# Kernel optimization log

Hardware: AMD Instinct MI355X
Metric: run time of the kernel (lower is better)

## Reference

```python
import jax, jax.numpy as jnp
import numpy as np
import math

EPS = 1e-5
N_HEADS = 4


def _ln(x, g, b):
    mu = jnp.mean(x, axis=-1, keepdims=True)
    var = jnp.mean((x - mu) ** 2, axis=-1, keepdims=True)
    return (x - mu) * jax.lax.rsqrt(var + EPS) * g + b


def _eq_ln(s, v, g, b, vscale):
    # scalar LayerNorm + equivariant vector norm rescaling
    s = _ln(s, g, b)
    vn = jnp.sqrt(jnp.sum(v * v, axis=-1, keepdims=True))  # (B,N,C,1)
    v = v / (vn + EPS) * jnp.mean(vn, axis=-2, keepdims=True) * vscale[None, None, :, None]
    return s, v


def _block(s, v, pos, Wq, bq, Wk, bk, Wv, bv, Wo, bo, w_dist, b_dist, Wvv, Wvo,
           g1, be1, vs1, g2, be2, vs2, Wf1, bf1, Wf2, bf2, Wfv1, Wfv2):
    B, N, S = s.shape
    D = S // N_HEADS
    # --- norm1 + attention ---
    sn, vn = _eq_ln(s, v, g1, be1, vs1)
    q = (sn @ Wq + bq).reshape(B, N, N_HEADS, D)
    k = (sn @ Wk + bk).reshape(B, N, N_HEADS, D)
    vs = (sn @ Wv + bv).reshape(B, N, N_HEADS, D)
    attn = jnp.einsum('bnhd,bmhd->bhnm', q, k) / math.sqrt(D)
    # pairwise Euclidean distance via the |x|^2 + |y|^2 - 2xy trick (clamped for sqrt safety)
    p2 = jnp.sum(pos * pos, axis=-1)  # (B,N)
    d2 = p2[:, :, None] + p2[:, None, :] - 2.0 * jnp.einsum('bnd,bmd->bnm', pos, pos)
    dist = jnp.sqrt(jnp.maximum(d2, 1e-12))  # (B,N,N)
    # dist_proj: Linear(1 -> n_heads) + Softplus, applied per pair
    bias = jax.nn.softplus(dist[..., None] * w_dist + b_dist)  # (B,N,N,H)
    attn = jax.nn.softmax(attn - jnp.transpose(bias, (0, 3, 1, 2)), axis=-1)  # (B,H,N,N)
    attn_mean = jnp.mean(attn, axis=1)  # (B,N,N)
    s_attn = jnp.einsum('bhnm,bmhd->bnhd', attn, vs).reshape(B, N, S) @ Wo + bo
    # vector channel mixing + rotation by head-averaged attention
    v_mix = jnp.einsum('bncx,ce->bnex', vn, Wvv)          # (B,N,C,3)
    v_attn = jnp.einsum('bnm,bmcx->bncx', attn_mean, v_mix)
    v_attn = jnp.einsum('bncx,ce->bnex', v_attn, Wvo)
    s = s + s_attn
    v = v + v_attn
    # --- norm2 + FFN ---
    sn, vn = _eq_ln(s, v, g2, be2, vs2)
    s = s + (jax.nn.gelu(sn @ Wf1 + bf1, approximate=False) @ Wf2 + bf2)
    v = v + jnp.einsum('bnhx,hc->bncx', jnp.einsum('bncx,ch->bnhx', vn, Wfv1), Wfv2)
    return s, v


def setup_inputs() -> dict:
    B, N, S, C, H = 4, 2048, 256, 64, N_HEADS
    key = jax.random.key(0)
    ks = jax.random.split(key, 24)

    def nrm(k, shape, scale=0.02):
        return jax.random.normal(k, shape, dtype=jnp.float32) * scale

    return {
        's': jax.random.normal(ks[0], (B, N, S), dtype=jnp.float32),
        'v': jax.random.normal(ks[1], (B, N, C, 3), dtype=jnp.float32),
        'pos': jax.random.normal(ks[2], (B, N, 3), dtype=jnp.float32),
        'Wq': nrm(ks[3], (S, S)), 'bq': nrm(ks[4], (S,)),
        'Wk': nrm(ks[5], (S, S)), 'bk': nrm(ks[6], (S,)),
        'Wv': nrm(ks[7], (S, S)), 'bv': nrm(ks[8], (S,)),
        'Wo': nrm(ks[9], (S, S)), 'bo': nrm(ks[10], (S,)),
        'w_dist': nrm(ks[11], (H,), 0.5), 'b_dist': nrm(ks[12], (H,), 0.5),
        'Wvv': nrm(ks[13], (C, C)), 'Wvo': nrm(ks[14], (C, C)),
        'g1': jnp.ones((S,), jnp.float32), 'be1': jnp.zeros((S,), jnp.float32),
        'vs1': jnp.ones((C,), jnp.float32),
        'g2': jnp.ones((S,), jnp.float32), 'be2': jnp.zeros((S,), jnp.float32),
        'vs2': jnp.ones((C,), jnp.float32),
        'Wf1': nrm(ks[15], (S, 4 * S)), 'bf1': nrm(ks[16], (4 * S,)),
        'Wf2': nrm(ks[17], (4 * S, S)), 'bf2': nrm(ks[18], (S,)),
        'Wfv1': nrm(ks[19], (C, 4 * C)), 'Wfv2': nrm(ks[20], (4 * C, C)),
    }


def reference(s, v, pos, Wq, bq, Wk, bk, Wv, bv, Wo, bo, w_dist, b_dist, Wvv, Wvo,
              g1, be1, vs1, g2, be2, vs2, Wf1, bf1, Wf2, bf2, Wfv1, Wfv2):
    return _block(s, v, pos, Wq, bq, Wk, bk, Wv, bv, Wo, bo, w_dist, b_dist, Wvv, Wvo,
                  g1, be1, vs1, g2, be2, vs2, Wf1, bf1, Wf2, bf2, Wfv1, Wfv2)
```

## Files before the change

### kernel.cpp

```cpp
#include <hip/hip_runtime.h>
#include <hip/hip_bf16.h>

using bf16 = __hip_bfloat16;
typedef __attribute__((ext_vector_type(8))) short short8;
typedef __attribute__((ext_vector_type(4))) float float4v;
typedef __attribute__((ext_vector_type(16))) float f32x16;
typedef __attribute__((ext_vector_type(4))) unsigned uint4v;

__device__ __forceinline__ float b2f(bf16 x){ return __bfloat162float(x); }
__device__ __forceinline__ bf16  f2b(float x){ return __float2bfloat16(x); }
__device__ __forceinline__ bf16  tob(float x){ return f2b(x); }
__device__ __forceinline__ bf16  tob(bf16 x){ return x; }
__device__ __forceinline__ float frcp(float x){ return __builtin_amdgcn_rcpf(x); }
__device__ __forceinline__ float bs2f(short s){
  unsigned u = ((unsigned)(unsigned short)s) << 16;
  return __builtin_bit_cast(float, u);
}
__device__ __forceinline__ unsigned cvt_pk_bf16(float lo, float hi){
  unsigned r; asm("v_cvt_pk_bf16_f32 %0, %1, %2" : "=v"(r) : "v"(lo), "v"(hi)); return r;
}
__device__ __forceinline__ void plswap(unsigned &a, unsigned &b){
  asm("v_permlane32_swap_b32 %0, %1" : "+v"(a), "+v"(b));
}

#define EPSV 1e-5f
#define Z16 {0.f,0.f,0.f,0.f,0.f,0.f,0.f,0.f,0.f,0.f,0.f,0.f,0.f,0.f,0.f,0.f}

__global__ __launch_bounds__(256) void pos_kernel(const float* __restrict__ pos,
                                                  float* __restrict__ posf, int rows){
  int r = blockIdx.x*256 + threadIdx.x;
  if (r >= rows) return;
  float x = pos[3*r], y = pos[3*r+1], z = pos[3*r+2];
  posf[4*r] = x; posf[4*r+1] = y; posf[4*r+2] = z; posf[4*r+3] = x*x + y*y + z*z;
}

struct WTDesc { const float* src; bf16* dst; int rows, cols; };
struct WTPack { WTDesc d[10]; };

__global__ __launch_bounds__(256) void wtrans_kernel(WTPack p){
  WTDesc w = p.d[blockIdx.z];
  long r0 = (long)blockIdx.y*32, c0 = (long)blockIdx.x*32;
  if (r0 >= w.rows || c0 >= w.cols) return;
  __shared__ bf16 tile[32][33];
  int tx = threadIdx.x & 31, ty = threadIdx.x >> 5;
#pragma unroll
  for (int i = ty; i < 32; i += 8) tile[i][tx] = f2b(w.src[(r0+i)*w.cols + c0 + tx]);
  __syncthreads();
#pragma unroll
  for (int i = ty; i < 32; i += 8) w.dst[(c0+i)*w.rows + r0 + tx] = tile[tx][i];
}

template<typename TI>
__global__ __launch_bounds__(256) void transpose_kernel(
    const TI* __restrict__ in, long ldin, long is1, long is2,
    bf16* __restrict__ out, long ldout, long os1, long os2, int Z2)
{
  int z = blockIdx.z, z1 = z / Z2, z2 = z - z1*Z2;
  in  += (long)z1*is1 + (long)z2*is2;
  out += (long)z1*os1 + (long)z2*os2;
  __shared__ bf16 tile[32][33];
  int tx = threadIdx.x & 31, ty = threadIdx.x >> 5;
  long r0 = (long)blockIdx.y*32, c0 = (long)blockIdx.x*32;
#pragma unroll
  for (int i = ty; i < 32; i += 8) tile[i][tx] = tob(in[(r0+i)*ldin + c0 + tx]);
  __syncthreads();
#pragma unroll
  for (int i = ty; i < 32; i += 8) out[(c0+i)*ldout + r0 + tx] = tile[tx][i];
}

__global__ __launch_bounds__(256) void bcat_kernel(const float* __restrict__ bq,
                                                   const float* __restrict__ bk,
                                                   const float* __restrict__ bv,
                                                   float* __restrict__ bqkv){
  int j = blockIdx.x*256 + threadIdx.x;
  if (j >= 768) return;
  bqkv[j] = (j < 256) ? bq[j] : (j < 512) ? bk[j-256] : bv[j-512];
}

__global__ __launch_bounds__(256) void ln_kernel(const float* __restrict__ x,
                                                 const float* __restrict__ g,
                                                 const float* __restrict__ be,
                                                 bf16* __restrict__ out){
  const long row = blockIdx.x;
  const int t = threadIdx.x;
  __shared__ float r1[256], r2[256];
  float v = x[(row<<8) + t];
  r1[t] = v; r2[t] = v*v; __syncthreads();
  for (int s=128;s>0;s>>=1){
    if (t<s){ r1[t] += r1[t+s]; r2[t] += r2[t+s]; }
    __syncthreads();
  }
  const float mu = r1[0] * (1.f/256.f);
  const float var = r2[0] * (1.f/256.f) - mu*mu;
  const float rstd = rsqrtf(fmaxf(var, 0.f) + EPSV);
  out[(row<<8)+t] = f2b((v-mu)*rstd*g[t] + be[t]);
}

__global__ __launch_bounds__(192) void vnorm1_kernel(const float* __restrict__ vin,
                                                     const float* __restrict__ vs1,
                                                     bf16* __restrict__ vnX){
  const long row = blockIdx.x;
  const int t = threadIdx.x;
  __shared__ float vv[192], nrm[64];
  __shared__ float smean;
  vv[t] = vin[row*192 + t];
  __syncthreads();
  if (t < 64){
    float a = vv[3*t], b = vv[3*t+1], c = vv[3*t+2];
    nrm[t] = sqrtf(a*a + b*b + c*c);
  }
  __syncthreads();
  if (t == 0){ float s = 0.f; for (int i=0;i<64;i++) s += nrm[i]; smean = s*(1.f/64.f); }
  __syncthreads();
  const int c = t/3, x = t - 3*c;
  const float val = vv[t] / (nrm[c] + EPSV) * smean * vs1[c];
  vnX[row*192 + x*64 + c] = f2b(val);
}

__global__ __launch_bounds__(192) void vnorm2_kernel(const float* __restrict__ v2X,
                                                     const float* __restrict__ vs2,
                                                     bf16* __restrict__ vn2X){
  const long row = blockIdx.x;
  const int t = threadIdx.x;
  __shared__ float vv[192], nrm[64];
  __shared__ float smean;
  vv[t] = v2X[row*192 + t];
  __syncthreads();
  if (t < 64){
    float a = vv[t], b = vv[t+64], c = vv[t+128];
    nrm[t] = sqrtf(a*a + b*b + c*c);
  }
  __syncthreads();
  if (t == 0){ float s = 0.f; for (int i=0;i<64;i++) s += nrm[i]; smean = s*(1.f/64.f); }
  __syncthreads();
  const int c = t & 63;
  vn2X[row*192 + t] = f2b(vv[t] / (nrm[c] + EPSV) * smean * vs2[c]);
}

__global__ __launch_bounds__(256) void knorm_kernel(const bf16* __restrict__ qkv,
                                                    float* __restrict__ kmax){
  const int bh = blockIdx.x, b = bh>>2, h = bh&3;
  const int t = threadIdx.x;
  __shared__ float red[256];
  float mx = 0.f;
  for (int r=0;r<8;r++){
    long row = (long)b*2048 + r*256 + t;
    const short8* kp = (const short8*)(qkv + row*768 + 256 + h*64);
    float ss = 0.f;
#pragma unroll
    for (int c=0;c<8;c++){
      short8 v = kp[c];
#pragma unroll
      for (int j=0;j<8;j++){ float f = bs2f(v[j]); ss = fmaf(f,f,ss); }
    }
    mx = fmaxf(mx, ss);
  }
  red[t] = mx; __syncthreads();
  for (int s=128;s>0;s>>=1){ if (t<s) red[t] = fmaxf(red[t], red[t+s]); __syncthreads(); }
  if (t==0) kmax[bh] = sqrtf(red[0]);
}

#define ATT_K_OFF   0
#define ATT_V_OFF   4096
#define ATT_X_OFF   9216
#define ATT_P_OFF   24576
#define ATT_TILE    25088
#define ATT_GRP     50176
#define ATT_LACC    98304
#define ATT_SMEM    100352

__global__ __launch_bounds__(512, 2) void attn_kernel(
    const bf16* __restrict__ qkv,
    const bf16* __restrict__ vsT,
    const bf16* __restrict__ vmixT,
    const float* __restrict__ posf,
    const float* __restrict__ kmaxA,
    const float* __restrict__ w_dist, const float* __restrict__ b_dist,
    bf16* __restrict__ sA,
    bf16* __restrict__ slab)
{
  __shared__ __align__(16) char smem[ATT_SMEM];
  const int qb = blockIdx.x;
  const int bh = blockIdx.y;
  const int b  = bh >> 2, h = bh & 3;
  const int tid = threadIdx.x;
  const int w = tid >> 6, lane = tid & 63;
  const int g = w >> 2, qw = w & 3;
  const int lq = lane & 31, hi = lane >> 5;
  const int gtid = tid & 255;

  const int qloc = qb*128 + qw*32 + lq;
  const long rowQ = (long)b*2048 + qloc;

  short8 qf[4];
  {
    const bf16* qp = qkv + rowQ*768 + h*64 + hi*8;
#pragma unroll
    for (int kc=0;kc<4;kc++) qf[kc] = *(const short8*)(qp + kc*16);
  }
  float q2 = 0.f;
#pragma unroll
  for (int kc=0;kc<4;kc++)
#pragma unroll
    for (int j=0;j<8;j++){ float qv = bs2f(qf[kc][j]); q2 = fmaf(qv,qv,q2); }
  q2 += __shfl_xor(q2, 32);
  const float mxs = sqrtf(q2) * kmaxA[bh] * 0.125f;
  const float wh = w_dist[h], bhd = b_dist[h];
  const float4v pn = *(const float4v*)(posf + (long)b*8192 + (long)qloc*4);
  const float m2x = -2.f*pn[0], m2y = -2.f*pn[1], m2z = -2.f*pn[2], pnw = pn[3];

  f32x16 O[2]  = {Z16, Z16};
  f32x16 VM[6] = {Z16, Z16, Z16, Z16, Z16, Z16};
  float lacc = 0.f;

  short8 stK, stV, stX0, stX1, stX2; float4v stP;
  const int sm = gtid >> 3, sc = gtid & 7;
  const int vd = gtid >> 2, vc = gtid & 3;
  const bf16* Kg = qkv + (long)b*2048*768 + 256 + h*64;
  const bf16* Vg = vsT + (long)b*524288 + (long)h*131072;
  const bf16* Xg = vmixT + (long)b*393216;
  const float* Pg = posf + (long)b*8192;
  char* gbase = smem + g*ATT_GRP;

  auto LOADT = [&](int m0){
    stK  = *(const short8*)(Kg + (long)(m0+sm)*768 + sc*8);
    stV  = *(const short8*)(Vg + (long)vd*2048 + m0 + vc*8);
    stX0 = *(const short8*)(Xg + (long)vd*2048 + m0 + vc*8);
    stX1 = *(const short8*)(Xg + (long)(64+vd)*2048 + m0 + vc*8);
    stX2 = *(const short8*)(Xg + (long)(128+vd)*2048 + m0 + vc*8);
    if (gtid < 32) stP = *(const float4v*)(Pg + (long)(m0+gtid)*4);
  };
  auto WRITET = [&](char* buf){
    *(short8*)(buf + ATT_K_OFF + sm*128 + ((sc ^ (sm&7))<<4)) = stK;
    *(short8*)(buf + ATT_V_OFF + vd*80 + vc*16) = stV;
    *(short8*)(buf + ATT_X_OFF + vd*80 + vc*16) = stX0;
    *(short8*)(buf + ATT_X_OFF + (64+vd)*80 + vc*16) = stX1;
    *(short8*)(buf + ATT_X_OFF + (128+vd)*80 + vc*16) = stX2;
    if (gtid < 32) *(float4v*)(buf + ATT_P_OFF + gtid*16) = stP;
  };

  auto COMPUTE = [&](const char* buf){
    const char* Kb = buf + ATT_K_OFF;
    const char* Vb = buf + ATT_V_OFF;
    const char* Xb = buf + ATT_X_OFF;
    const float4v* pmb = (const float4v*)(buf + ATT_P_OFF);
    f32x16 S = Z16;
#pragma unroll
    for (int kc=0;kc<4;kc++){
      short8 kf = *(const short8*)(Kb + lq*128 + (((kc*2+hi) ^ (lq&7))<<4));
      S = __builtin_amdgcn_mfma_f32_32x32x16_bf16(kf, qf[kc], S, 0, 0, 0);
    }
    float P[16];
#pragma unroll
    for (int gg=0; gg<4; gg++){
#pragma unroll
      for (int i=0;i<4;i++){
        float4v pm = pmb[gg*8 + hi*4 + i];
        float d2 = fmaf(m2x, pm[0], fmaf(m2y, pm[1], fmaf(m2z, pm[2], pnw + pm[3])));
        float dist = sqrtf(fmaxf(d2, 1e-12f));
        float sig = frcp(1.f + __expf(fmaf(dist, wh, bhd)));
        float p = __expf(fmaf(S[gg*4+i], 0.125f, -mxs)) * sig;
        lacc += p;
        P[gg*4+i] = p;
      }
    }
    unsigned pk[8];
#pragma unroll
    for (int t=0;t<8;t++) pk[t] = cvt_pk_bf16(P[2*t], P[2*t+1]);
    plswap(pk[0], pk[2]); plswap(pk[1], pk[3]);
    plswap(pk[4], pk[6]); plswap(pk[5], pk[7]);
    uint4v y0v = {pk[0], pk[1], pk[2], pk[3]};
    uint4v y1v = {pk[4], pk[5], pk[6], pk[7]};
    short8 Y0 = __builtin_bit_cast(short8, y0v);
    short8 Y1 = __builtin_bit_cast(short8, y1v);
#pragma unroll
    for (int dblk=0; dblk<2; dblk++){
      short8 v0 = *(const short8*)(Vb + (dblk*32+lq)*80 + hi*16);
      short8 v1 = *(const short8*)(Vb + (dblk*32+lq)*80 + 32 + hi*16);
      O[dblk] = __builtin_amdgcn_mfma_f32_32x32x16_bf16(v0, Y0, O[dblk], 0,0,0);
      O[dblk] = __builtin_amdgcn_mfma_f32_32x32x16_bf16(v1, Y1, O[dblk], 0,0,0);
    }
#pragma unroll
    for (int eblk=0; eblk<6; eblk++){
      short8 x0 = *(const short8*)(Xb + (eblk*32+lq)*80 + hi*16);
      short8 x1 = *(const short8*)(Xb + (eblk*32+lq)*80 + 32 + hi*16);
      VM[eblk] = __builtin_amdgcn_mfma_f32_32x32x16_bf16(x0, Y0, VM[eblk], 0,0,0);
      VM[eblk] = __builtin_amdgcn_mfma_f32_32x32x16_bf16(x1, Y1, VM[eblk], 0,0,0);
    }
  };

  LOADT(g*32);
  WRITET(gbase);
  __syncthreads();
#pragma unroll 1
  for (int i=0; i<32; ++i){
    if (i < 31) LOADT((2*(i+1)+g)*32);
    COMPUTE(gbase + (i&1)*ATT_TILE);
    if (i < 31) WRITET(gbase + ((i+1)&1)*ATT_TILE);
    __syncthreads();
  }

  float* laccT = (float*)(smem + ATT_LACC);
  laccT[w*64 + lane] = lacc;
  if (g == 1){
    float* Od = (float*)(smem + ATT_GRP) + (qw*64+lane)*33;
#pragma unroll
    for (int r=0;r<16;r++){ Od[r] = O[0][r]; Od[16+r] = O[1][r]; }
  }
  __syncthreads();
  const float lsum = laccT[qw*64+lq] + laccT[qw*64+32+lq]
                   + laccT[(4+qw)*64+lq] + laccT[(4+qw)*64+32+lq];
  if (g == 0){
    const float* Od = (const float*)(smem + ATT_GRP) + (qw*64+lane)*33;
#pragma unroll
    for (int r=0;r<16;r++){ O[0][r] += Od[r]; O[1][r] += Od[16+r]; }
  }
  __syncthreads();
#pragma unroll
  for (int hf=0; hf<2; hf++){
    if (g == 0){
      float* Vd = (float*)smem + (qw*64+lane)*49;
#pragma unroll
      for (int e=0;e<3;e++)
#pragma unroll
        for (int r=0;r<16;r++) Vd[e*16+r] = VM[hf*3+e][r];
    }
    __syncthreads();
    if (g == 1){
      const float* Vd = (const float*)smem + (qw*64+lane)*49;
#pragma unroll
      for (int e=0;e<3;e++)
#pragma unroll
        for (int r=0;r<16;r++) VM[hf*3+e][r] += Vd[e*16+r];
    }
    __syncthreads();
  }

  const float sinv = frcp(lsum);
  if (g == 0){
    char* scr = smem + qw*12544;
#pragma unroll
    for (int dblk=0; dblk<2; dblk++)
#pragma unroll
      for (int pp=0; pp<8; pp++){
        const int r = 2*pp;
        const int d = dblk*32 + (r&3) + 8*(r>>2) + 4*hi;
        unsigned u = cvt_pk_bf16(O[dblk][r]*sinv, O[dblk][r+1]*sinv);
        *(unsigned*)(scr + lq*136 + d*2) = u;
      }
  } else {
    const float vinv = 0.25f * sinv;
    char* scr = smem + ATT_GRP + qw*12544;
#pragma unroll
    for (int eblk=0; eblk<6; eblk++)
#pragma unroll
      for (int pp=0; pp<8; pp++){
        const int r = 2*pp;
        const int e = eblk*32 + (r&3) + 8*(r>>2) + 4*hi;
        unsigned u = cvt_pk_bf16(VM[eblk][r]*vinv, VM[eblk][r+1]*vinv);
        *(unsigned*)(scr + lq*392 + e*2) = u;
      }
  }
  __syncthreads();
  if (g == 0){
    const char* scr = smem + qw*12544;
    const int q = lane >> 1, half = lane & 1;
    const char* src = scr + q*136 + half*64;
    char* dst = (char*)(sA + (long)(b*2048 + qb*128 + qw*32 + q)*256 + h*64 + half*32);
#pragma unroll
    for (int i=0;i<8;i++)
      *(unsigned long long*)(dst + i*8) = *(const unsigned long long*)(src + i*8);
  } else {
    const char* scr = smem + ATT_GRP + qw*12544;
    const int q = lane >> 1, half = lane & 1;
    const char* src = scr + q*392 + half*192;
    char* dst = (char*)(slab + (long)h*1572864
                        + (long)(b*2048 + qb*128 + qw*32 + q)*192 + half*96);
#pragma unroll
    for (int i=0;i<24;i++)
      *(unsigned long long*)(dst + i*8) = *(const unsigned long long*)(src + i*8);
  }
}

__global__ __launch_bounds__(256) void hred_kernel(const bf16* __restrict__ slab,
                                                   bf16* __restrict__ out){
  long i = (long)blockIdx.x*256 + threadIdx.x;
  if (i >= 196608) return;
  const short8* s0 = (const short8*)slab + i;
  short8 a = s0[0], b = s0[196608], c = s0[2*196608], d = s0[3*196608];
  short8 o;
#pragma unroll
  for (int j=0;j<8;j++){
    float f = bs2f(a[j]) + bs2f(b[j]) + bs2f(c[j]) + bs2f(d[j]);
    bf16 hv = f2b(f); o[j] = *(short*)&hv;
  }
  ((short8*)out)[i] = o;
}

template<int MT, int NT, int ACT, int OUTM, int RXIL, int CXIL, int SWZ>
__global__ __launch_bounds__(64) void gemm_kernel(
    const bf16* __restrict__ A, long lda, long As1, long As2,
    const bf16* __restrict__ BT, long ldb, long Bs1, long Bs2,
    const float* __restrict__ bias,
    const float* __restrict__ resid, long ldr, long Rs1, long Rs2,
    void* __restrict__ Cv, long ldc, long Cs1, long Cs2,
    int K, int Z2, int KS)
{
  int z = blockIdx.z;
  int zz = z / KS, ks = z - zz*KS;
  int z1 = zz / Z2, z2 = zz - z1*Z2;
  A  += (long)z1*As1 + (long)z2*As2 + (long)ks*K;
  BT += (long)z1*Bs1 + (long)z2*Bs2 + (long)ks*K;
  if (resid) resid += (long)z1*Rs1 + (long)z2*Rs2;
  const long cbase = (long)z1*Cs1 + (long)z2*Cs2;

  int bx = blockIdx.x, by = blockIdx.y;
  if (SWZ){
    const int nx = gridDim.x, ny = gridDim.y;
    long lin = (long)by*nx + bx;
    const int xcd = (int)(lin & 7);
    long idx = lin >> 3;
    const int rpx = ny >> 3;
    by = xcd*rpx + (int)(idx / nx);
    bx = (int)(idx % nx);
  }

  const int lane = threadIdx.x;
  const int col = lane & 15, quad = lane >> 4;
  const long rowA0 = (long)by*(16*MT);
  const long colB0 = (long)bx*(16*NT);

  float4v acc[MT][NT];
#pragma unroll
  for (int m=0;m<MT;m++)
#pragma unroll
    for (int n=0;n<NT;n++) acc[m][n] = (float4v){0.f,0.f,0.f,0.f};

  const bf16* ap[MT];
  const bf16* bp[NT];
#pragma unroll
  for (int m=0;m<MT;m++) ap[m] = A + (rowA0 + m*16 + col)*lda + quad*8;
#pragma unroll
  for (int n=0;n<NT;n++) bp[n] = BT + (colB0 + n*16 + col)*ldb + quad*8;

  for (int k0 = 0; k0 < K; k0 += 32){
    short8 a[MT], bb[NT];
#pragma unroll
    for (int m=0;m<MT;m++){ a[m] = *(const short8*)ap[m]; ap[m] += 32; }
#pragma unroll
    for (int n=0;n<NT;n++){ bb[n] = *(const short8*)bp[n]; bp[n] += 32; }
#pragma unroll
    for (int m=0;m<MT;m++)
#pragma unroll
      for (int n=0;n<NT;n++)
        acc[m][n] = __builtin_amdgcn_mfma_f32_16x16x32_bf16(a[m], bb[n], acc[m][n], 0, 0, 0);
  }

#pragma unroll
  for (int m=0;m<MT;m++){
    const long ri = rowA0 + m*16 + quad*4;
#pragma unroll
    for (int n=0;n<NT;n++){
      const long cj = colB0 + n*16 + col;
      const float bbias = bias ? bias[cj] : 0.f;
#pragma unroll
      for (int r=0;r<4;r++){
        const long ci = ri + r;
        float val = acc[m][n][r] + bbias;
        if (ACT == 1) val = 0.5f*val*(1.f + erff(val*0.70710678118654752f));
        if (resid){
          const long raddr = RXIL ? ((ci/3)*192 + cj*3 + (ci%3)) : (ci*ldr + cj);
          val += resid[raddr];
        }
        const long caddr = CXIL ? (cbase + (ci/3)*192 + cj*3 + (ci%3))
                                : (cbase + ci*ldc + cj);
        if (OUTM == 0)      ((bf16*)Cv)[caddr] = f2b(val);
        else if (OUTM == 1) ((float*)Cv)[caddr] = val;
        else                unsafeAtomicAdd(&((float*)Cv)[caddr], val);
      }
    }
  }
}

extern "C" void kernel_launch(void* const* d_in, const int* in_sizes, int n_in,
                              void* d_out, int out_size, void* d_ws, size_t ws_size,
                              hipStream_t stream)
{
  const float* s    = (const float*)d_in[0];
  const float* v    = (const float*)d_in[1];
  const float* pos  = (const float*)d_in[2];
  const float* Wq   = (const float*)d_in[3];
  const float* bq   = (const float*)d_in[4];
  const float* Wk   = (const float*)d_in[5];
  const float* bk   = (const float*)d_in[6];
  const float* Wv   = (const float*)d_in[7];
  const float* bv   = (const float*)d_in[8];
  const float* Wo   = (const float*)d_in[9];
  const float* bo   = (const float*)d_in[10];
  const float* w_d  = (const float*)d_in[11];
  const float* b_d  = (const float*)d_in[12];
  const float* Wvv  = (const float*)d_in[13];
  const float* Wvo  = (const float*)d_in[14];
  const float* g1   = (const float*)d_in[15];
  const float* be1  = (const float*)d_in[16];
  const float* vs1  = (const float*)d_in[17];
  const float* g2   = (const float*)d_in[18];
  const float* be2  = (const float*)d_in[19];
  const float* vs2  = (const float*)d_in[20];
  const float* Wf1  = (const float*)d_in[21];
  const float* bf1  = (const float*)d_in[22];
  const float* Wf2  = (const float*)d_in[23];
  const float* bf2  = (const float*)d_in[24];
  const float* Wfv1 = (const float*)d_in[25];
  const float* Wfv2 = (const float*)d_in[26];

  float* outS = (float*)d_out;
  float* outV = outS + (size_t)4*2048*256;

  char* w = (char*)d_ws;
  size_t o = 0;
  auto alloc = [&](size_t bytes)->char* {
    char* p = w + o;
    o = (o + bytes + 255) & ~(size_t)255;
    return p;
  };
  float* posf  = (float*)alloc(131072);
  bf16* WqkvT = (bf16*)alloc(393216);
  bf16* WoT   = (bf16*)alloc(131072);
  bf16* Wf1T  = (bf16*)alloc(524288);
  bf16* Wf2T  = (bf16*)alloc(524288);
  bf16* WvvT  = (bf16*)alloc(8192);
  bf16* WvoT  = (bf16*)alloc(8192);
  bf16* Wfv1T = (bf16*)alloc(32768);
  bf16* Wfv2T = (bf16*)alloc(32768);
  float* bqkv = (float*)alloc(3072);
  float* kmax = (float*)alloc(64);
  bf16* sn    = (bf16*)alloc(4194304);
  bf16* qkv   = (bf16*)alloc(12582912);
  bf16* vsT   = (bf16*)alloc(4194304);
  bf16* sA    = (bf16*)alloc(4194304);
  float* s2   = (float*)alloc(8388608);
  bf16* vnX   = (bf16*)alloc(3145728);
  bf16* vmixX = (bf16*)alloc(3145728);
  bf16* vmixXT= (bf16*)alloc(3145728);
  float* v2X  = (float*)alloc(6291456);
  bf16* slab  = (bf16*)alloc(12582912);
  bf16* h1    = (bf16*)alloc(16777216);
  bf16* vn2X  = vnX;
  bf16* tvXb  = vmixX;
  bf16* hv    = qkv;
  if (o > ws_size) return;

  pos_kernel<<<32, 256, 0, stream>>>(pos, posf, 8192);
  WTPack pk;
  pk.d[0] = {Wq,   WqkvT,          256, 256};
  pk.d[1] = {Wk,   WqkvT + 65536,  256, 256};
  pk.d[2] = {Wv,   WqkvT + 131072, 256, 256};
  pk.d[3] = {Wo,   WoT,            256, 256};
  pk.d[4] = {Wf1,  Wf1T,           256, 1024};
  pk.d[5] = {Wf2,  Wf2T,           1024, 256};
  pk.d[6] = {Wvv,  WvvT,           64, 64};
  pk.d[7] = {Wvo,  WvoT,           64, 64};
  pk.d[8] = {Wfv1, Wfv1T,          64, 256};
  pk.d[9] = {Wfv2, Wfv2T,          256, 64};
  wtrans_kernel<<<dim3(32,32,10), 256, 0, stream>>>(pk);
  bcat_kernel<<<3, 256, 0, stream>>>(bq, bk, bv, bqkv);

  ln_kernel<<<8192, 256, 0, stream>>>(s, g1, be1, sn);
  vnorm1_kernel<<<8192, 192, 0, stream>>>(v, vs1, vnX);

  gemm_kernel<2,4,0,0,0,0,0><<<dim3(1,768,1), 64, 0, stream>>>(vnX,64,0,0, WvvT,64,0,0,
      nullptr, nullptr,0,0,0, vmixX,64,0,0, 64, 1, 1);
  transpose_kernel<bf16><<<dim3(6,64,4), 256, 0, stream>>>(vmixX, 192, 393216,0,
      vmixXT, 2048, 393216,0, 1);

  gemm_kernel<2,4,0,0,0,0,1><<<dim3(12,256,1), 64, 0, stream>>>(sn,256,0,0, WqkvT,256,0,0,
      bqkv, nullptr,0,0,0, qkv,768,0,0, 256, 1, 1);
  transpose_kernel<bf16><<<dim3(2,64,16), 256, 0, stream>>>(qkv+512, 768, 1572864,64,
      vsT, 2048, 524288,131072, 4);

  knorm_kernel<<<16, 256, 0, stream>>>(qkv, kmax);
  attn_kernel<<<dim3(16,16), 512, 0, stream>>>(qkv, vsT, vmixXT, posf, kmax,
      w_d, b_d, sA, slab);
  hred_kernel<<<768, 256, 0, stream>>>(slab, tvXb);

  gemm_kernel<2,4,0,1,0,0,1><<<dim3(4,256,1), 64, 0, stream>>>(sA,256,0,0, WoT,256,0,0,
      bo, s,256,0,0, s2,256,0,0, 256, 1, 1);

  gemm_kernel<2,4,0,1,1,0,0><<<dim3(1,768,1), 64, 0, stream>>>(tvXb,64,0,0, WvoT,64,0,0,
      nullptr, v,0,0,0, v2X,64,0,0, 64, 1, 1);

  ln_kernel<<<8192, 256, 0, stream>>>(s2, g2, be2, sn);
  gemm_kernel<2,4,1,0,0,0,1><<<dim3(16,256,1), 64, 0, stream>>>(sn,256,0,0, Wf1T,256,0,0,
      bf1, nullptr,0,0,0, h1,1024,0,0, 256, 1, 1);
  gemm_kernel<2,4,0,1,0,0,1><<<dim3(4,256,1), 64, 0, stream>>>(h1,1024,0,0, Wf2T,1024,0,0,
      bf2, s2,256,0,0, outS,256,0,0, 1024, 1, 1);

  vnorm2_kernel<<<8192, 192, 0, stream>>>(v2X, vs2, vn2X);
  gemm_kernel<2,4,0,0,0,0,1><<<dim3(4,768,1), 64, 0, stream>>>(vn2X,64,0,0, Wfv1T,64,0,0,
      nullptr, nullptr,0,0,0, hv,256,0,0, 64, 1, 1);
  gemm_kernel<2,4,0,1,0,1,0><<<dim3(1,768,1), 64, 0, stream>>>(hv,256,0,0, Wfv2T,256,0,0,
      nullptr, v2X,64,0,0, outV,0,0,0, 256, 1, 1);
}
```

Measured before the change: 425.9 us.

## Shrink attention blocks, single-buffer tiles, parallelize knorm, enlarge GEMM tiles

The attention kernel moves from 512-thread blocks of 128 queries with double-buffered shared tiles to 256-thread blocks of 64 queries with a single buffer. This halves shared memory per block so more blocks can be resident, at the cost of an extra barrier per iteration and less load/compute overlap. The key-norm reduction is split across 8 row chunks per head and combined with an atomic max on squared norms, which are zeroed in the bias-concat kernel; the square root moves into the attention kernel. All GEMM launches switch to a larger M tile template parameter with half as many blocks.

```diff
diff --git a/kernel.cpp b/kernel.cpp
--- a/kernel.cpp
+++ b/kernel.cpp
@@ -71,8 +71,10 @@
 __global__ __launch_bounds__(256) void bcat_kernel(const float* __restrict__ bq,
                                                    const float* __restrict__ bk,
                                                    const float* __restrict__ bv,
-                                                   float* __restrict__ bqkv){
+                                                   float* __restrict__ bqkv,
+                                                   float* __restrict__ kmax){
   int j = blockIdx.x*256 + threadIdx.x;
+  if (blockIdx.x == 0 && threadIdx.x < 16) kmax[threadIdx.x] = 0.f;
   if (j >= 768) return;
   bqkv[j] = (j < 256) ? bq[j] : (j < 512) ? bk[j-256] : bv[j-512];
 }
@@ -142,22 +144,18 @@
   const int bh = blockIdx.x, b = bh>>2, h = bh&3;
   const int t = threadIdx.x;
   __shared__ float red[256];
-  float mx = 0.f;
-  for (int r=0;r<8;r++){
-    long row = (long)b*2048 + r*256 + t;
-    const short8* kp = (const short8*)(qkv + row*768 + 256 + h*64);
-    float ss = 0.f;
-#pragma unroll
-    for (int c=0;c<8;c++){
-      short8 v = kp[c];
-#pragma unroll
-      for (int j=0;j<8;j++){ float f = bs2f(v[j]); ss = fmaf(f,f,ss); }
-    }
-    mx = fmaxf(mx, ss);
-  }
-  red[t] = mx; __syncthreads();
+  long row = (long)b*2048 + (long)blockIdx.y*256 + t;
+  const short8* kp = (const short8*)(qkv + row*768 + 256 + h*64);
+  float ss = 0.f;
+#pragma unroll
+  for (int c=0;c<8;c++){
+    short8 v = kp[c];
+#pragma unroll
+    for (int j=0;j<8;j++){ float f = bs2f(v[j]); ss = fmaf(f,f,ss); }
+  }
+  red[t] = ss; __syncthreads();
   for (int s=128;s>0;s>>=1){ if (t<s) red[t] = fmaxf(red[t], red[t+s]); __syncthreads(); }
-  if (t==0) kmax[bh] = sqrtf(red[0]);
+  if (t==0) atomicMax((unsigned*)&kmax[bh], __float_as_uint(red[0]));
 }
 
 #define ATT_K_OFF   0
@@ -165,11 +163,10 @@
 #define ATT_X_OFF   9216
 #define ATT_P_OFF   24576
 #define ATT_TILE    25088
-#define ATT_GRP     50176
-#define ATT_LACC    98304
-#define ATT_SMEM    100352
-
-__global__ __launch_bounds__(512, 2) void attn_kernel(
+#define ATT_LACC    50176
+#define ATT_SMEM    51200
+
+__global__ __launch_bounds__(256, 3) void attn_kernel(
     const bf16* __restrict__ qkv,
     const bf16* __restrict__ vsT,
     const bf16* __restrict__ vmixT,
@@ -185,11 +182,11 @@
   const int b  = bh >> 2, h = bh & 3;
   const int tid = threadIdx.x;
   const int w = tid >> 6, lane = tid & 63;
-  const int g = w >> 2, qw = w & 3;
+  const int g = w >> 1, qw = w & 1;
   const int lq = lane & 31, hi = lane >> 5;
-  const int gtid = tid & 255;
-
-  const int qloc = qb*128 + qw*32 + lq;
+  const int gt = tid & 127;
+
+  const int qloc = qb*64 + qw*32 + lq;
   const long rowQ = (long)b*2048 + qloc;
 
   short8 qf[4];
@@ -204,7 +201,7 @@
 #pragma unroll
     for (int j=0;j<8;j++){ float qv = bs2f(qf[kc][j]); q2 = fmaf(qv,qv,q2); }
   q2 += __shfl_xor(q2, 32);
-  const float mxs = sqrtf(q2) * kmaxA[bh] * 0.125f;
+  const float mxs = sqrtf(q2 * kmaxA[bh]) * 0.125f;
   const float wh = w_dist[h], bhd = b_dist[h];
   const float4v pn = *(const float4v*)(posf + (long)b*8192 + (long)qloc*4);
   const float m2x = -2.f*pn[0], m2y = -2.f*pn[1], m2z = -2.f*pn[2], pnw = pn[3];
@@ -213,30 +210,38 @@
   f32x16 VM[6] = {Z16, Z16, Z16, Z16, Z16, Z16};
   float lacc = 0.f;
 
-  short8 stK, stV, stX0, stX1, stX2; float4v stP;
-  const int sm = gtid >> 3, sc = gtid & 7;
-  const int vd = gtid >> 2, vc = gtid & 3;
+  short8 stK[2], stV[2], stX[6]; float4v stP;
   const bf16* Kg = qkv + (long)b*2048*768 + 256 + h*64;
   const bf16* Vg = vsT + (long)b*524288 + (long)h*131072;
   const bf16* Xg = vmixT + (long)b*393216;
   const float* Pg = posf + (long)b*8192;
-  char* gbase = smem + g*ATT_GRP;
+  char* gbase = smem + g*ATT_TILE;
 
   auto LOADT = [&](int m0){
-    stK  = *(const short8*)(Kg + (long)(m0+sm)*768 + sc*8);
-    stV  = *(const short8*)(Vg + (long)vd*2048 + m0 + vc*8);
-    stX0 = *(const short8*)(Xg + (long)vd*2048 + m0 + vc*8);
-    stX1 = *(const short8*)(Xg + (long)(64+vd)*2048 + m0 + vc*8);
-    stX2 = *(const short8*)(Xg + (long)(128+vd)*2048 + m0 + vc*8);
-    if (gtid < 32) stP = *(const float4v*)(Pg + (long)(m0+gtid)*4);
+#pragma unroll
+    for (int c=0;c<2;c++)
+      stK[c] = *(const short8*)(Kg + (long)(m0 + (gt>>3) + 16*c)*768 + (gt&7)*8);
+#pragma unroll
+    for (int c=0;c<2;c++)
+      stV[c] = *(const short8*)(Vg + (long)((gt>>2) + 32*c)*2048 + m0 + (gt&3)*8);
+#pragma unroll
+    for (int c=0;c<6;c++)
+      stX[c] = *(const short8*)(Xg + (long)((gt>>2) + 32*c)*2048 + m0 + (gt&3)*8);
+    if (gt < 32) stP = *(const float4v*)(Pg + (long)(m0+gt)*4);
   };
   auto WRITET = [&](char* buf){
-    *(short8*)(buf + ATT_K_OFF + sm*128 + ((sc ^ (sm&7))<<4)) = stK;
-    *(short8*)(buf + ATT_V_OFF + vd*80 + vc*16) = stV;
-    *(short8*)(buf + ATT_X_OFF + vd*80 + vc*16) = stX0;
-    *(short8*)(buf + ATT_X_OFF + (64+vd)*80 + vc*16) = stX1;
-    *(short8*)(buf + ATT_X_OFF + (128+vd)*80 + vc*16) = stX2;
-    if (gtid < 32) *(float4v*)(buf + ATT_P_OFF + gtid*16) = stP;
+#pragma unroll
+    for (int c=0;c<2;c++){
+      const int r = (gt>>3) + 16*c;
+      *(short8*)(buf + ATT_K_OFF + r*128 + (((gt&7) ^ (r&7))<<4)) = stK[c];
+    }
+#pragma unroll
+    for (int c=0;c<2;c++)
+      *(short8*)(buf + ATT_V_OFF + ((gt>>2)+32*c)*80 + (gt&3)*16) = stV[c];
+#pragma unroll
+    for (int c=0;c<6;c++)
+      *(short8*)(buf + ATT_X_OFF + ((gt>>2)+32*c)*80 + (gt&3)*16) = stX[c];
+    if (gt < 32) *(float4v*)(buf + ATT_P_OFF + gt*16) = stP;
   };
 
   auto COMPUTE = [&](const char* buf){
@@ -295,23 +300,26 @@
 #pragma unroll 1
   for (int i=0; i<32; ++i){
     if (i < 31) LOADT((2*(i+1)+g)*32);
-    COMPUTE(gbase + (i&1)*ATT_TILE);
-    if (i < 31) WRITET(gbase + ((i+1)&1)*ATT_TILE);
+    COMPUTE(gbase);
     __syncthreads();
+    if (i < 31){
+      WRITET(gbase);
+      __syncthreads();
+    }
   }
 
   float* laccT = (float*)(smem + ATT_LACC);
   laccT[w*64 + lane] = lacc;
   if (g == 1){
-    float* Od = (float*)(smem + ATT_GRP) + (qw*64+lane)*33;
+    float* Od = (float*)smem + (qw*64+lane)*33;
 #pragma unroll
     for (int r=0;r<16;r++){ Od[r] = O[0][r]; Od[16+r] = O[1][r]; }
   }
   __syncthreads();
   const float lsum = laccT[qw*64+lq] + laccT[qw*64+32+lq]
-                   + laccT[(4+qw)*64+lq] + laccT[(4+qw)*64+32+lq];
+                   + laccT[(2+qw)*64+lq] + laccT[(2+qw)*64+32+lq];
   if (g == 0){
-    const float* Od = (const float*)(smem + ATT_GRP) + (qw*64+lane)*33;
+    const float* Od = (const float*)smem + (qw*64+lane)*33;
 #pragma unroll
     for (int r=0;r<16;r++){ O[0][r] += Od[r]; O[1][r] += Od[16+r]; }
   }
@@ -338,7 +346,7 @@
 
   const float sinv = frcp(lsum);
   if (g == 0){
-    char* scr = smem + qw*12544;
+    char* scr = smem + qw*4352;
 #pragma unroll
     for (int dblk=0; dblk<2; dblk++)
 #pragma unroll
@@ -350,7 +358,7 @@
       }
   } else {
     const float vinv = 0.25f * sinv;
-    char* scr = smem + ATT_GRP + qw*12544;
+    char* scr = smem + 8704 + qw*12544;
 #pragma unroll
     for (int eblk=0; eblk<6; eblk++)
 #pragma unroll
@@ -363,19 +371,19 @@
   }
   __syncthreads();
   if (g == 0){
-    const char* scr = smem + qw*12544;
+    const char* scr = smem + qw*4352;
     const int q = lane >> 1, half = lane & 1;
     const char* src = scr + q*136 + half*64;
-    char* dst = (char*)(sA + (long)(b*2048 + qb*128 + qw*32 + q)*256 + h*64 + half*32);
+    char* dst = (char*)(sA + (long)(b*2048 + qb*64 + qw*32 + q)*256 + h*64 + half*32);
 #pragma unroll
     for (int i=0;i<8;i++)
       *(unsigned long long*)(dst + i*8) = *(const unsigned long long*)(src + i*8);
   } else {
-    const char* scr = smem + ATT_GRP + qw*12544;
+    const char* scr = smem + 8704 + qw*12544;
     const int q = lane >> 1, half = lane & 1;
     const char* src = scr + q*392 + half*192;
     char* dst = (char*)(slab + (long)h*1572864
-                        + (long)(b*2048 + qb*128 + qw*32 + q)*192 + half*96);
+                        + (long)(b*2048 + qb*64 + qw*32 + q)*192 + half*96);
 #pragma unroll
     for (int i=0;i<24;i++)
       *(unsigned long long*)(dst + i*8) = *(const unsigned long long*)(src + i*8);
@@ -564,41 +572,41 @@
   pk.d[8] = {Wfv1, Wfv1T,          64, 256};
   pk.d[9] = {Wfv2, Wfv2T,          256, 64};
   wtrans_kernel<<<dim3(32,32,10), 256, 0, stream>>>(pk);
-  bcat_kernel<<<3, 256, 0, stream>>>(bq, bk, bv, bqkv);
+  bcat_kernel<<<3, 256, 0, stream>>>(bq, bk, bv, bqkv, kmax);
 
   ln_kernel<<<8192, 256, 0, stream>>>(s, g1, be1, sn);
   vnorm1_kernel<<<8192, 192, 0, stream>>>(v, vs1, vnX);
 
-  gemm_kernel<2,4,0,0,0,0,0><<<dim3(1,768,1), 64, 0, stream>>>(vnX,64,0,0, WvvT,64,0,0,
+  gemm_kernel<4,4,0,0,0,0,0><<<dim3(1,384,1), 64, 0, stream>>>(vnX,64,0,0, WvvT,64,0,0,
       nullptr, nullptr,0,0,0, vmixX,64,0,0, 64, 1, 1);
   transpose_kernel<bf16><<<dim3(6,64,4), 256, 0, stream>>>(vmixX, 192, 393216,0,
       vmixXT, 2048, 393216,0, 1);
 
-  gemm_kernel<2,4,0,0,0,0,1><<<dim3(12,256,1), 64, 0, stream>>>(sn,256,0,0, WqkvT,256,0,0,
+  gemm_kernel<4,4,0,0,0,0,1><<<dim3(12,128,1), 64, 0, stream>>>(sn,256,0,0, WqkvT,256,0,0,
       bqkv, nullptr,0,0,0, qkv,768,0,0, 256, 1, 1);
   transpose_kernel<bf16><<<dim3(2,64,16), 256, 0, stream>>>(qkv+512, 768, 1572864,64,
       vsT, 2048, 524288,131072, 4);
 
-  knorm_kernel<<<16, 256, 0, stream>>>(qkv, kmax);
-  attn_kernel<<<dim3(16,16), 512, 0, stream>>>(qkv, vsT, vmixXT, posf, kmax,
+  knorm_kernel<<<dim3(16,8), 256, 0, stream>>>(qkv, kmax);
+  attn_kernel<<<dim3(32,16), 256, 0, stream>>>(qkv, vsT, vmixXT, posf, kmax,
       w_d, b_d, sA, slab);
   hred_kernel<<<768, 256, 0, stream>>>(slab, tvXb);
 
-  gemm_kernel<2,4,0,1,0,0,1><<<dim3(4,256,1), 64, 0, stream>>>(sA,256,0,0, WoT,256,0,0,
+  gemm_kernel<4,4,0,1,0,0,1><<<dim3(4,128,1), 64, 0, stream>>>(sA,256,0,0, WoT,256,0,0,
       bo, s,256,0,0, s2,256,0,0, 256, 1, 1);
 
-  gemm_kernel<2,4,0,1,1,0,0><<<dim3(1,768,1), 64, 0, stream>>>(tvXb,64,0,0, WvoT,64,0,0,
+  gemm_kernel<4,4,0,1,1,0,0><<<dim3(1,384,1), 64, 0, stream>>>(tvXb,64,0,0, WvoT,64,0,0,
       nullptr, v,0,0,0, v2X,64,0,0, 64, 1, 1);
 
   ln_kernel<<<8192, 256, 0, stream>>>(s2, g2, be2, sn);
-  gemm_kernel<2,4,1,0,0,0,1><<<dim3(16,256,1), 64, 0, stream>>>(sn,256,0,0, Wf1T,256,0,0,
+  gemm_kernel<4,4,1,0,0,0,1><<<dim3(16,128,1), 64, 0, stream>>>(sn,256,0,0, Wf1T,256,0,0,
       bf1, nullptr,0,0,0, h1,1024,0,0, 256, 1, 1);
-  gemm_kernel<2,4,0,1,0,0,1><<<dim3(4,256,1), 64, 0, stream>>>(h1,1024,0,0, Wf2T,1024,0,0,
+  gemm_kernel<4,4,0,1,0,0,1><<<dim3(4,128,1), 64, 0, stream>>>(h1,1024,0,0, Wf2T,1024,0,0,
       bf2, s2,256,0,0, outS,256,0,0, 1024, 1, 1);
 
   vnorm2_kernel<<<8192, 192, 0, stream>>>(v2X, vs2, vn2X);
-  gemm_kernel<2,4,0,0,0,0,1><<<dim3(4,768,1), 64, 0, stream>>>(vn2X,64,0,0, Wfv1T,64,0,0,
+  gemm_kernel<4,4,0,0,0,0,1><<<dim3(4,384,1), 64, 0, stream>>>(vn2X,64,0,0, Wfv1T,64,0,0,
       nullptr, nullptr,0,0,0, hv,256,0,0, 64, 1, 1);
-  gemm_kernel<2,4,0,1,0,1,0><<<dim3(1,768,1), 64, 0, stream>>>(hv,256,0,0, Wfv2T,256,0,0,
+  gemm_kernel<4,4,0,1,0,1,0><<<dim3(1,384,1), 64, 0, stream>>>(hv,256,0,0, Wfv2T,256,0,0,
       nullptr, v2X,64,0,0, outV,0,0,0, 256, 1, 1);
 }
```

After: 1.099 ms. +158.1%, slower.
